# Kernel tuning notes

Measured on AMD Instinct MI355X. Metric: run time of the kernel, lower is better.

Reference implementation:

```python
import jax, jax.numpy as jnp
import numpy as np

IN_DIM = 128
OUT_DIM = 128
NUM_INTERVALS = 8
SPLINE_ORDER = 3
BATCH = 1024


def make_grids():
    # domain [-1, 1] for every (in, out) pair, extended by spline_order knots each side
    step = 2.0 / NUM_INTERVALS
    G = NUM_INTERVALS + 2 * SPLINE_ORDER + 1
    g = (-1.0 - SPLINE_ORDER * step) + jnp.arange(G, dtype=jnp.float32) * step  # [G]
    return jnp.broadcast_to(g, (IN_DIM, OUT_DIM, G))


def setup_inputs() -> dict:
    key = jax.random.key(0)
    k1, k2, k3 = jax.random.split(key, 3)
    x = jax.random.normal(k1, (BATCH, IN_DIM), dtype=jnp.float32)
    n_cp = NUM_INTERVALS + SPLINE_ORDER
    control_points = 0.1 * jax.random.normal(k2, (IN_DIM, OUT_DIM, n_cp), dtype=jnp.float32)
    scaling_factors = np.sqrt(2.0 / OUT_DIM).astype(np.float32) * jax.random.normal(
        k3, (IN_DIM, OUT_DIM), dtype=jnp.float32)
    grids = make_grids()
    return {"x": x, "control_points": control_points,
            "scaling_factors": scaling_factors, "grids": grids}


def bspline_bases(x, grids, k):
    # Bottom-up Cox-de-Boor DP (identical recurrence to the naive top-down version).
    # x: [B, in], grids: [in, out, G] -> returns all degree-k bases [B, in, out, G-1-k]
    ex = x[:, :, None, None]          # [B, in, 1, 1]
    t = grids[None]                   # [1, in, out, G]
    B = ((t[..., :-1] <= ex) & (ex < t[..., 1:])).astype(x.dtype)  # degree 0
    for d in range(1, k + 1):
        tl  = t[..., : -(d + 1)]      # t[i]
        tr  = t[..., d:-1]            # t[i+d]
        tl1 = t[..., 1:-d]            # t[i+1]
        tr1 = t[..., d + 1:]          # t[i+d+1]
        B = (ex - tl) / (tr - tl) * B[..., :-1] + (tr1 - ex) / (tr1 - tl1) * B[..., 1:]
    return B


def reference(x, control_points, scaling_factors, grids):
    Bk = bspline_bases(x, grids, SPLINE_ORDER)                 # [B, in, out, n_cp]
    spline = jnp.einsum('biog,iog->bio', Bk, control_points)    # [B, in, out]
    res = scaling_factors[None] * (jax.nn.silu(x)[:, :, None] + spline)
    return jnp.sum(res, axis=1).astype(jnp.float32)             # [B, out]
```

## Files before the change

### kernel.cpp

```cpp
#include <hip/hip_runtime.h>
#include <math.h>


#define IN_DIM   128
#define OUT_DIM  128
#define NCP      11
#define GK       15
#define FS       12
#define KTOT     (IN_DIM * FS)
#define BT       8
#define OT       32
#define VO       4
#define KSP      64
#define NJ       (KTOT / 4 / KSP)
#define THREADS  512
#define RPAD     260

__global__ __launch_bounds__(256)
void kan_prep(const float* __restrict__ CP,
              const float* __restrict__ SF,
              float* __restrict__ W)
{
    const int p = blockIdx.x * 256 + threadIdx.x;
    const int i = p >> 7;
    const int o = p & (OUT_DIM - 1);
    const float s = SF[p];
    const float* cp = CP + p * NCP;
    const int kb = i * FS;
    #pragma unroll
    for (int g = 0; g < NCP; ++g)
        W[(kb + g) * OUT_DIM + o] = s * cp[g];
    W[(kb + NCP) * OUT_DIM + o] = s;
}

__global__ __launch_bounds__(THREADS, 2)
void kan_main(const float* __restrict__ X,
              const float* __restrict__ GR,
              const float* __restrict__ W,
              float* __restrict__ OUT)
{
    __shared__ float S[KSP * RPAD];

    const int tid = threadIdx.x;
    const int b0  = blockIdx.x * BT;
    const int o0  = blockIdx.y * OT;

    const float t0 = GR[0];
    const float h  = GR[1] - t0;
    const float r1 = 1.0f / h;
    const float r2 = 1.0f / (2.0f * h);
    const float r3 = 1.0f / (3.0f * h);
    float kn[GK];
    #pragma unroll
    for (int j = 0; j < GK; ++j) kn[j] = t0 + (float)j * h;

    float* F = S;
    #pragma unroll
    for (int kq = 0; kq < (BT * IN_DIM) / THREADS; ++kq) {
        const int p = tid + kq * THREADS;
        const int r = p >> 7;
        const int i = p & (IN_DIM - 1);

        const float x = X[(b0 + r) * IN_DIM + i];

        float b[GK - 1];
        #pragma unroll
        for (int j = 0; j < GK - 1; ++j)
            b[j] = (kn[j] <= x && x < kn[j + 1]) ? 1.0f : 0.0f;
        #pragma unroll
        for (int j = 0; j < GK - 2; ++j)
            b[j] = ((x - kn[j]) * b[j] + (kn[j + 2] - x) * b[j + 1]) * r1;
        #pragma unroll
        for (int j = 0; j < GK - 3; ++j)
            b[j] = ((x - kn[j]) * b[j] + (kn[j + 3] - x) * b[j + 1]) * r2;
        #pragma unroll
        for (int j = 0; j < GK - 4; ++j)
            b[j] = ((x - kn[j]) * b[j] + (kn[j + 4] - x) * b[j + 1]) * r3;

        const float silu = x / (1.0f + __expf(-x));

        float* f = &F[p * FS];
        *(float4*)(f + 0) = make_float4(b[0], b[1], b[2], b[3]);
        *(float4*)(f + 4) = make_float4(b[4], b[5], b[6], b[7]);
        *(float4*)(f + 8) = make_float4(b[8], b[9], b[10], silu);
    }
    __syncthreads();

    const int ol = tid & (OT / VO - 1);
    const int ks = tid >> 3;
    const int o4 = o0 + VO * ol;

    float acc[BT][VO];
    #pragma unroll
    for (int r = 0; r < BT; ++r)
        #pragma unroll
        for (int v = 0; v < VO; ++v) acc[r][v] = 0.0f;

    #pragma unroll
    for (int j = 0; j < NJ; ++j) {
        const int kg = 4 * (ks + KSP * j);

        float4 w0 = *(const float4*)&W[(kg + 0) * OUT_DIM + o4];
        float4 w1 = *(const float4*)&W[(kg + 1) * OUT_DIM + o4];
        float4 w2 = *(const float4*)&W[(kg + 2) * OUT_DIM + o4];
        float4 w3 = *(const float4*)&W[(kg + 3) * OUT_DIM + o4];

        #pragma unroll
        for (int r = 0; r < BT; ++r) {
            const float4 f = *(const float4*)&F[r * KTOT + kg];
            acc[r][0] = fmaf(f.x, w0.x, acc[r][0]);
            acc[r][1] = fmaf(f.x, w0.y, acc[r][1]);
            acc[r][2] = fmaf(f.x, w0.z, acc[r][2]);
            acc[r][3] = fmaf(f.x, w0.w, acc[r][3]);
            acc[r][0] = fmaf(f.y, w1.x, acc[r][0]);
            acc[r][1] = fmaf(f.y, w1.y, acc[r][1]);
            acc[r][2] = fmaf(f.y, w1.z, acc[r][2]);
            acc[r][3] = fmaf(f.y, w1.w, acc[r][3]);
            acc[r][0] = fmaf(f.z, w2.x, acc[r][0]);
            acc[r][1] = fmaf(f.z, w2.y, acc[r][1]);
            acc[r][2] = fmaf(f.z, w2.z, acc[r][2]);
            acc[r][3] = fmaf(f.z, w2.w, acc[r][3]);
            acc[r][0] = fmaf(f.w, w3.x, acc[r][0]);
            acc[r][1] = fmaf(f.w, w3.y, acc[r][1]);
            acc[r][2] = fmaf(f.w, w3.z, acc[r][2]);
            acc[r][3] = fmaf(f.w, w3.w, acc[r][3]);
        }
    }

    __syncthreads();
    float* red = S;
    #pragma unroll
    for (int r = 0; r < BT; ++r)
        *(float4*)&red[ks * RPAD + r * OT + VO * ol] =
            make_float4(acc[r][0], acc[r][1], acc[r][2], acc[r][3]);
    __syncthreads();

    if (tid < BT * OT) {
        const int r  = tid >> 5;
        const int oc = tid & 31;
        float v = 0.0f;
        #pragma unroll
        for (int q = 0; q < KSP; ++q)
            v += red[q * RPAD + r * OT + oc];
        OUT[(b0 + r) * OUT_DIM + o0 + oc] = v;
    }
}

extern "C" void kernel_launch(void* const* d_in, const int* in_sizes, int n_in,
                              void* d_out, int out_size, void* d_ws, size_t ws_size,
                              hipStream_t stream) {
    const float* x  = (const float*)d_in[0];
    const float* cp = (const float*)d_in[1];
    const float* sf = (const float*)d_in[2];
    const float* gr = (const float*)d_in[3];
    float* out = (float*)d_out;
    float* W   = (float*)d_ws;

    const int batch = in_sizes[0] / IN_DIM;

    kan_prep<<<(IN_DIM * OUT_DIM) / 256, 256, 0, stream>>>(cp, sf, W);
    dim3 grid(batch / BT, OUT_DIM / OT);
    kan_main<<<grid, THREADS, 0, stream>>>(x, gr, W, out);
}
```

Baseline: 71.91 us.

## Double batch tile per block and coalesce weight-prep via shared memory

Raises the batch rows per block from 8 to 16, so each weight float4 loaded from global memory is reused across twice as many rows. This also halves the block count and roughly doubles shared-memory use, with the padded reduction buffer grown to match. That likely cuts residency to one block per CU. The prep kernel now runs one block per input dimension: it stages control points and scaling factors in LDS with float4 loads, then writes W in a coalesced pattern instead of making strided per-thread reads.

```diff
diff --git a/kernel.cpp b/kernel.cpp
--- a/kernel.cpp
+++ b/kernel.cpp
@@ -8,29 +8,40 @@
 #define GK       15
 #define FS       12
 #define KTOT     (IN_DIM * FS)
-#define BT       8
+#define BT       16
 #define OT       32
 #define VO       4
 #define KSP      64
 #define NJ       (KTOT / 4 / KSP)
 #define THREADS  512
-#define RPAD     260
+#define RPAD     516
 
 __global__ __launch_bounds__(256)
 void kan_prep(const float* __restrict__ CP,
               const float* __restrict__ SF,
               float* __restrict__ W)
 {
-    const int p = blockIdx.x * 256 + threadIdx.x;
-    const int i = p >> 7;
-    const int o = p & (OUT_DIM - 1);
-    const float s = SF[p];
-    const float* cp = CP + p * NCP;
-    const int kb = i * FS;
+    __shared__ float cpL[IN_DIM * NCP];
+    __shared__ float sfL[OUT_DIM];
+
+    const int i = blockIdx.x;
+    const int t = threadIdx.x;
+
+    const float4* src = (const float4*)(CP + i * OUT_DIM * NCP);
     #pragma unroll
-    for (int g = 0; g < NCP; ++g)
-        W[(kb + g) * OUT_DIM + o] = s * cp[g];
-    W[(kb + NCP) * OUT_DIM + o] = s;
+    for (int q = t; q < (OUT_DIM * NCP) / 4; q += 256)
+        ((float4*)cpL)[q] = src[q];
+    if (t < OUT_DIM) sfL[t] = SF[i * OUT_DIM + t];
+    __syncthreads();
+
+    #pragma unroll
+    for (int e = t; e < FS * OUT_DIM; e += 256) {
+        const int g = e >> 7;
+        const int o = e & (OUT_DIM - 1);
+        const float s = sfL[o];
+        const float w = (g < NCP) ? s * cpL[o * NCP + g] : s;
+        W[(i * FS + g) * OUT_DIM + o] = w;
+    }
 }
 
 __global__ __launch_bounds__(THREADS, 2)
@@ -135,7 +146,7 @@
             make_float4(acc[r][0], acc[r][1], acc[r][2], acc[r][3]);
     __syncthreads();
 
-    if (tid < BT * OT) {
+    {
         const int r  = tid >> 5;
         const int oc = tid & 31;
         float v = 0.0f;
@@ -158,7 +169,7 @@
 
     const int batch = in_sizes[0] / IN_DIM;
 
-    kan_prep<<<(IN_DIM * OUT_DIM) / 256, 256, 0, stream>>>(cp, sf, W);
+    kan_prep<<<IN_DIM, 256, 0, stream>>>(cp, sf, W);
     dim3 grid(batch / BT, OUT_DIM / OT);
     kan_main<<<grid, THREADS, 0, stream>>>(x, gr, W, out);
 }
```

After: 76.27 us. 1.06x slower.
